# Optimization experiments

Hardware: AMD Instinct MI355X
Metric: run time of the kernel (lower is better)

The kernel has to match this reference:

```python
import jax, jax.numpy as jnp
import numpy as np

NUM_ROUTING = 3
EPS = 1e-8


def squash(s, axis=-1):
    # v = ||s||^2/(1+||s||^2) * s/||s||
    sq = jnp.sum(s * s, axis=axis, keepdims=True)
    return sq / (1.0 + sq) * s / (jnp.sqrt(sq) + EPS)


def setup_inputs() -> dict:
    key = jax.random.key(0)
    k1, k2 = jax.random.split(key)
    batch, in_caps, in_dim = 16, 2048, 64
    num_caps, dim_caps = 64, 32
    x = jax.random.normal(k1, (batch, in_caps, in_dim), dtype=jnp.float32)
    # learned transform W[j, d, k]  (torch shape (1,num_caps,1,dim_caps,in_dim) with singletons dropped)
    W = 0.01 * jax.random.normal(k2, (num_caps, dim_caps, in_dim), dtype=jnp.float32)
    return {"x": x, "W": W}


def reference(x, W):
    # u_hat[b,j,i,d] = sum_k W[j,d,k] * x[b,i,k]
    u_hat = jnp.einsum('jdk,bik->bjid', W, x)  # (b, num_caps, in_caps, dim_caps)
    u_hat_d = jax.lax.stop_gradient(u_hat)     # routing uses detached predictions

    b = jnp.zeros(u_hat.shape[:3] + (1,), dtype=u_hat.dtype)  # (b, J, I, 1)
    for _ in range(NUM_ROUTING - 1):
        c = jax.nn.softmax(b, axis=1)                # over output capsules J
        s = jnp.sum(c * u_hat_d, axis=2)             # (b, J, D)
        v = squash(s)
        # agreement uv[b,j,i] = <u_hat_d[b,j,i,:], v[b,j,:]>
        b = b + jnp.einsum('bjid,bjd->bji', u_hat_d, v)[..., None]

    c = jax.nn.softmax(b, axis=1)
    s = jnp.sum(c * u_hat, axis=2)
    return squash(s)  # (b, num_caps, dim_caps)
```

## Files before the change

kernel.cpp:

```cpp
#include <hip/hip_runtime.h>
#include <math.h>


#define BB 16
#define II 2048
#define KK 64
#define JJ 64
#define DD 32
#define ITILE 64
#define NT (II / ITILE)
#define YB 16

__global__ __launch_bounds__(256) void ybar_kernel(const float* __restrict__ x,
                                                   float* __restrict__ ybarp) {
    const int b = blockIdx.x;
    const int q = blockIdx.y;
    const int tid = threadIdx.x;
    const int kq = tid & 15;
    const int r  = tid >> 4;
    const float4* xp = (const float4*)(x + ((size_t)b * II + (size_t)q * 128) * KK) + kq;
    float4 a = make_float4(0.f, 0.f, 0.f, 0.f);
    #pragma unroll
    for (int n = 0; n < 8; ++n) {
        const float4 v = xp[(size_t)(r + n * 16) * 16];
        a.x += v.x; a.y += v.y; a.z += v.z; a.w += v.w;
    }
    __shared__ float4 sm[16][17];
    sm[r][kq] = a;
    __syncthreads();
    if (tid < 64) {
        const float* smf = (const float*)sm;
        float s = 0.f;
        #pragma unroll
        for (int rr = 0; rr < 16; ++rr) s += smf[rr * 68 + tid];
        ybarp[(b * YB + q) * KK + tid] = s * (1.0f / 64.0f);
    }
}

template <int MODE>
__global__ __launch_bounds__(256) void caps_kernel(const float* __restrict__ W,
                                                   const float* __restrict__ ybarp,
                                                   const float* __restrict__ ypart,
                                                   float* __restrict__ wv,
                                                   float* __restrict__ out) {
    const int b = blockIdx.x;
    const int jq = blockIdx.y;
    const int tid = threadIdx.x;
    const int w = tid >> 6;
    const int lane = tid & 63;
    const int j = jq * 4 + w;

    __shared__ alignas(16) float W_sm[4][DD][68];
    __shared__ alignas(16) float y_sm[4][KK];
    __shared__ float v_sm[4][DD];

    const float* Wp = W + (size_t)j * DD * KK;
    #pragma unroll
    for (int rr = 0; rr < 8; ++rr) {
        const int idx = rr * 64 + lane;
        const int d = idx >> 4, kq = idx & 15;
        *(float4*)&W_sm[w][d][kq * 4] = *(const float4*)(Wp + d * KK + kq * 4);
    }

    if (MODE == 0) {
        const float* yp = ybarp + (size_t)b * YB * KK + lane;
        float a = 0.f;
        #pragma unroll
        for (int t = 0; t < YB; ++t) a += yp[(size_t)t * KK];
        y_sm[w][lane] = a;
    } else {
        const int kq = lane & 15, th = lane >> 4;
        float4 a = make_float4(0.f, 0.f, 0.f, 0.f);
        #pragma unroll
        for (int n = 0; n < 8; ++n) {
            const int t = th + n * 4;
            const float4 v = *(const float4*)(ypart +
                (((size_t)b * NT + t) * JJ + j) * KK + kq * 4);
            a.x += v.x; a.y += v.y; a.z += v.z; a.w += v.w;
        }
        a.x += __shfl_xor(a.x, 16, 64); a.y += __shfl_xor(a.y, 16, 64);
        a.z += __shfl_xor(a.z, 16, 64); a.w += __shfl_xor(a.w, 16, 64);
        a.x += __shfl_xor(a.x, 32, 64); a.y += __shfl_xor(a.y, 32, 64);
        a.z += __shfl_xor(a.z, 32, 64); a.w += __shfl_xor(a.w, 32, 64);
        if (lane < 16) *(float4*)&y_sm[w][kq * 4] = a;
    }

    const int d = lane & 31;
    const int kh = (lane >> 5) * 32;
    float sv = 0.f;
    #pragma unroll
    for (int kq = 0; kq < 8; ++kq) {
        const float4 wr = *(const float4*)&W_sm[w][d][kh + kq * 4];
        const float4 yr = *(const float4*)&y_sm[w][kh + kq * 4];
        sv += wr.x * yr.x + wr.y * yr.y + wr.z * yr.z + wr.w * yr.w;
    }
    sv += __shfl_xor(sv, 32, 64);

    float ps = sv * sv;
    #pragma unroll
    for (int m = 1; m < 32; m <<= 1) ps += __shfl_xor(ps, m, 64);
    const float f = ps / ((1.f + ps) * (sqrtf(ps) + 1e-8f));

    if (MODE == 2) {
        if (lane < DD) out[((size_t)b * JJ + j) * DD + lane] = sv * f;
    } else {
        if (lane < DD) v_sm[w][lane] = sv * f;
        float a = 0.f;
        #pragma unroll
        for (int dd = 0; dd < DD; ++dd) a += W_sm[w][dd][lane] * v_sm[w][dd];
        const size_t idx = ((size_t)b * JJ + j) * KK + lane;
        if (MODE == 1) a += wv[idx];
        wv[idx] = a;
    }
}

__global__ __launch_bounds__(256) void route_kernel(const float* __restrict__ x,
                                                    const float* __restrict__ wv,
                                                    float* __restrict__ ypart) {
    const int b = blockIdx.x;
    const int t = blockIdx.y;
    const int tid = threadIdx.x;
    const int i0 = t * ITILE;

    __shared__ alignas(16) float x_smT[KK][68];
    __shared__ alignas(16) float wv_smT[KK][68];
    __shared__ alignas(16) float uv_smT[JJ][68];
    __shared__ float red[8][72];

    const float4* x4 = (const float4*)(x + ((size_t)b * II + i0) * KK);
    #pragma unroll
    for (int n = 0; n < 4; ++n) {
        const int idx = tid + n * 256;
        const int i = idx >> 4, kq = idx & 15;
        const float4 v = x4[idx];
        x_smT[kq * 4 + 0][i] = v.x;
        x_smT[kq * 4 + 1][i] = v.y;
        x_smT[kq * 4 + 2][i] = v.z;
        x_smT[kq * 4 + 3][i] = v.w;
    }
    const float4* wv4 = (const float4*)(wv + (size_t)b * JJ * KK);
    #pragma unroll
    for (int n = 0; n < 4; ++n) {
        const int idx = tid + n * 256;
        const int jj = idx >> 4, kq = idx & 15;
        const float4 v = wv4[idx];
        wv_smT[kq * 4 + 0][jj] = v.x;
        wv_smT[kq * 4 + 1][jj] = v.y;
        wv_smT[kq * 4 + 2][jj] = v.z;
        wv_smT[kq * 4 + 3][jj] = v.w;
    }
    __syncthreads();

    {
        const int ib = (tid & 15) * 4, jb = (tid >> 4) * 4;
        float acc[4][4] = {};
        for (int k = 0; k < KK; ++k) {
            const float4 xv = *(const float4*)&x_smT[k][ib];
            const float4 wvv = *(const float4*)&wv_smT[k][jb];
            acc[0][0] += xv.x * wvv.x; acc[0][1] += xv.x * wvv.y;
            acc[0][2] += xv.x * wvv.z; acc[0][3] += xv.x * wvv.w;
            acc[1][0] += xv.y * wvv.x; acc[1][1] += xv.y * wvv.y;
            acc[1][2] += xv.y * wvv.z; acc[1][3] += xv.y * wvv.w;
            acc[2][0] += xv.z * wvv.x; acc[2][1] += xv.z * wvv.y;
            acc[2][2] += xv.z * wvv.z; acc[2][3] += xv.z * wvv.w;
            acc[3][0] += xv.w * wvv.x; acc[3][1] += xv.w * wvv.y;
            acc[3][2] += xv.w * wvv.z; acc[3][3] += xv.w * wvv.w;
        }
        #pragma unroll
        for (int r = 0; r < 4; ++r)
            *(float4*)&uv_smT[jb + r][ib] =
                make_float4(acc[0][r], acc[1][r], acc[2][r], acc[3][r]);
    }
    __syncthreads();

    {
        const int i = tid & 63;
        const int w = tid >> 6;
        const int j0 = w * 16;
        float e[16];
        float m = -1e30f;
        #pragma unroll
        for (int jj = 0; jj < 16; ++jj) {
            e[jj] = uv_smT[j0 + jj][i];
            m = fmaxf(m, e[jj]);
        }
        red[w][i] = m;
        __syncthreads();
        m = fmaxf(fmaxf(red[0][i], red[1][i]), fmaxf(red[2][i], red[3][i]));
        float s = 0.f;
        #pragma unroll
        for (int jj = 0; jj < 16; ++jj) {
            e[jj] = __expf(e[jj] - m);
            s += e[jj];
        }
        red[4 + w][i] = s;
        __syncthreads();
        const float inv = 1.f / (red[4][i] + red[5][i] + red[6][i] + red[7][i]);
        #pragma unroll
        for (int jj = 0; jj < 16; ++jj) uv_smT[j0 + jj][i] = e[jj] * inv;
    }
    __syncthreads();

    {
        const int a = tid & 15;
        const int kb = (tid >> 4) * 4;
        float acc[4][4] = {};
        for (int i = 0; i < ITILE; i += 4) {
            float4 xv[4];
            #pragma unroll
            for (int c = 0; c < 4; ++c) xv[c] = *(const float4*)&x_smT[kb + c][i];
            #pragma unroll
            for (int r = 0; r < 4; ++r) {
                const float4 cv = *(const float4*)&uv_smT[a + 16 * r][i];
                #pragma unroll
                for (int c = 0; c < 4; ++c)
                    acc[r][c] += cv.x * xv[c].x + cv.y * xv[c].y +
                                 cv.z * xv[c].z + cv.w * xv[c].w;
            }
        }
        float* yp = ypart + ((size_t)b * NT + t) * JJ * KK;
        #pragma unroll
        for (int r = 0; r < 4; ++r)
            *(float4*)&yp[(a + 16 * r) * KK + kb] =
                make_float4(acc[r][0], acc[r][1], acc[r][2], acc[r][3]);
    }
}

extern "C" void kernel_launch(void* const* d_in, const int* in_sizes, int n_in,
                              void* d_out, int out_size, void* d_ws, size_t ws_size,
                              hipStream_t stream) {
    const float* x = (const float*)d_in[0];
    const float* W = (const float*)d_in[1];
    float* out = (float*)d_out;
    float* ws = (float*)d_ws;

    float* wv    = ws;
    float* ybarp = ws + 65536;
    float* ypart = ws + 65536 + 16384;

    ybar_kernel<<<dim3(BB, YB), 256, 0, stream>>>(x, ybarp);
    caps_kernel<0><<<dim3(BB, 16), 256, 0, stream>>>(W, ybarp, ypart, wv, out);
    route_kernel<<<dim3(BB, NT), 256, 0, stream>>>(x, wv, ypart);
    caps_kernel<1><<<dim3(BB, 16), 256, 0, stream>>>(W, ybarp, ypart, wv, out);
    route_kernel<<<dim3(BB, NT), 256, 0, stream>>>(x, wv, ypart);
    caps_kernel<2><<<dim3(BB, 16), 256, 0, stream>>>(W, ybarp, ypart, wv, out);
}
```

Baseline: 96.71 us.

## Use bf16 MFMA for routing GEMMs with in-register softmax

Rewrites route_kernel so both small GEMMs (agreement logits x·wv and c^T·x) run on bf16 16x16x32 MFMA instructions instead of scalar FP32 FMA loops. x and wv are converted to bf16 in shared memory, and x is kept in both row and transposed layouts. The softmax over the 64 output capsules is done in registers with cross-lane shuffles, which drops two barriers and the shared reduction buffer. In exchange, routing logits and coupling coefficients are computed in bf16, which lowers precision, and the final ypart stores are scalar with a strided pattern.

New measurement: 82.03 us. 15.2% less time.

```diff
diff --git a/kernel.cpp b/kernel.cpp
--- a/kernel.cpp
+++ b/kernel.cpp
@@ -10,6 +10,15 @@
 #define ITILE 64
 #define NT (II / ITILE)
 #define YB 16
+
+typedef float f32x4 __attribute__((ext_vector_type(4)));
+typedef short bf16x8 __attribute__((ext_vector_type(8)));
+
+__device__ __forceinline__ unsigned short f2bf(float f) {
+    unsigned int u = __float_as_uint(f);
+    u += 0x7FFFu + ((u >> 16) & 1u);
+    return (unsigned short)(u >> 16);
+}
 
 __global__ __launch_bounds__(256) void ybar_kernel(const float* __restrict__ x,
                                                    float* __restrict__ ybarp) {
@@ -114,121 +123,121 @@
     }
 }
 
-__global__ __launch_bounds__(256) void route_kernel(const float* __restrict__ x,
-                                                    const float* __restrict__ wv,
-                                                    float* __restrict__ ypart) {
+#define RPAD 72
+
+__global__ __launch_bounds__(256, 4) void route_kernel(const float* __restrict__ x,
+                                                       const float* __restrict__ wv,
+                                                       float* __restrict__ ypart) {
     const int b = blockIdx.x;
     const int t = blockIdx.y;
     const int tid = threadIdx.x;
-    const int i0 = t * ITILE;
-
-    __shared__ alignas(16) float x_smT[KK][68];
-    __shared__ alignas(16) float wv_smT[KK][68];
-    __shared__ alignas(16) float uv_smT[JJ][68];
-    __shared__ float red[8][72];
-
-    const float4* x4 = (const float4*)(x + ((size_t)b * II + i0) * KK);
+    const int w = tid >> 6;
+    const int lr = tid & 15;
+    const int lg = (tid >> 4) & 3;
+
+    __shared__ unsigned short x_bf[64][RPAD];
+    __shared__ unsigned short xT_bf[64][RPAD];
+    __shared__ unsigned short wv_bf[64][RPAD];
+    __shared__ unsigned short c_bf[64][RPAD];
+
+    const float4* x4 = (const float4*)(x + ((size_t)b * II + t * ITILE) * KK);
     #pragma unroll
     for (int n = 0; n < 4; ++n) {
         const int idx = tid + n * 256;
         const int i = idx >> 4, kq = idx & 15;
         const float4 v = x4[idx];
-        x_smT[kq * 4 + 0][i] = v.x;
-        x_smT[kq * 4 + 1][i] = v.y;
-        x_smT[kq * 4 + 2][i] = v.z;
-        x_smT[kq * 4 + 3][i] = v.w;
+        const unsigned short b0 = f2bf(v.x), b1 = f2bf(v.y),
+                             b2 = f2bf(v.z), b3 = f2bf(v.w);
+        *(unsigned int*)&x_bf[i][kq * 4 + 0] = (unsigned int)b0 | ((unsigned int)b1 << 16);
+        *(unsigned int*)&x_bf[i][kq * 4 + 2] = (unsigned int)b2 | ((unsigned int)b3 << 16);
+        xT_bf[kq * 4 + 0][i] = b0;
+        xT_bf[kq * 4 + 1][i] = b1;
+        xT_bf[kq * 4 + 2][i] = b2;
+        xT_bf[kq * 4 + 3][i] = b3;
     }
     const float4* wv4 = (const float4*)(wv + (size_t)b * JJ * KK);
     #pragma unroll
     for (int n = 0; n < 4; ++n) {
         const int idx = tid + n * 256;
-        const int jj = idx >> 4, kq = idx & 15;
+        const int j = idx >> 4, kq = idx & 15;
         const float4 v = wv4[idx];
-        wv_smT[kq * 4 + 0][jj] = v.x;
-        wv_smT[kq * 4 + 1][jj] = v.y;
-        wv_smT[kq * 4 + 2][jj] = v.z;
-        wv_smT[kq * 4 + 3][jj] = v.w;
+        *(unsigned int*)&wv_bf[j][kq * 4 + 0] =
+            (unsigned int)f2bf(v.x) | ((unsigned int)f2bf(v.y) << 16);
+        *(unsigned int*)&wv_bf[j][kq * 4 + 2] =
+            (unsigned int)f2bf(v.z) | ((unsigned int)f2bf(v.w) << 16);
     }
     __syncthreads();
 
+    f32x4 acc[4] = {{0,0,0,0},{0,0,0,0},{0,0,0,0},{0,0,0,0}};
     {
-        const int ib = (tid & 15) * 4, jb = (tid >> 4) * 4;
-        float acc[4][4] = {};
-        for (int k = 0; k < KK; ++k) {
-            const float4 xv = *(const float4*)&x_smT[k][ib];
-            const float4 wvv = *(const float4*)&wv_smT[k][jb];
-            acc[0][0] += xv.x * wvv.x; acc[0][1] += xv.x * wvv.y;
-            acc[0][2] += xv.x * wvv.z; acc[0][3] += xv.x * wvv.w;
-            acc[1][0] += xv.y * wvv.x; acc[1][1] += xv.y * wvv.y;
-            acc[1][2] += xv.y * wvv.z; acc[1][3] += xv.y * wvv.w;
-            acc[2][0] += xv.z * wvv.x; acc[2][1] += xv.z * wvv.y;
-            acc[2][2] += xv.z * wvv.z; acc[2][3] += xv.z * wvv.w;
-            acc[3][0] += xv.w * wvv.x; acc[3][1] += xv.w * wvv.y;
-            acc[3][2] += xv.w * wvv.z; acc[3][3] += xv.w * wvv.w;
-        }
+        const bf16x8 a0 = *(const bf16x8*)&x_bf[16 * w + lr][lg * 8];
+        const bf16x8 a1 = *(const bf16x8*)&x_bf[16 * w + lr][32 + lg * 8];
+        #pragma unroll
+        for (int jt = 0; jt < 4; ++jt) {
+            const bf16x8 bf0 = *(const bf16x8*)&wv_bf[jt * 16 + lr][lg * 8];
+            const bf16x8 bf1 = *(const bf16x8*)&wv_bf[jt * 16 + lr][32 + lg * 8];
+            acc[jt] = __builtin_amdgcn_mfma_f32_16x16x32_bf16(a0, bf0, acc[jt], 0, 0, 0);
+            acc[jt] = __builtin_amdgcn_mfma_f32_16x16x32_bf16(a1, bf1, acc[jt], 0, 0, 0);
+        }
+    }
+
+    float c[4][4];
+    #pragma unroll
+    for (int r = 0; r < 4; ++r) {
+        float m = fmaxf(fmaxf(acc[0][r], acc[1][r]), fmaxf(acc[2][r], acc[3][r]));
+        m = fmaxf(m, __shfl_xor(m, 1, 64));
+        m = fmaxf(m, __shfl_xor(m, 2, 64));
+        m = fmaxf(m, __shfl_xor(m, 4, 64));
+        m = fmaxf(m, __shfl_xor(m, 8, 64));
+        const float e0 = __expf(acc[0][r] - m);
+        const float e1 = __expf(acc[1][r] - m);
+        const float e2 = __expf(acc[2][r] - m);
+        const float e3 = __expf(acc[3][r] - m);
+        float s = e0 + e1 + e2 + e3;
+        s += __shfl_xor(s, 1, 64);
+        s += __shfl_xor(s, 2, 64);
+        s += __shfl_xor(s, 4, 64);
+        s += __shfl_xor(s, 8, 64);
+        const float inv = 1.f / s;
+        c[0][r] = e0 * inv; c[1][r] = e1 * inv;
+        c[2][r] = e2 * inv; c[3][r] = e3 * inv;
+    }
+
+    #pragma unroll
+    for (int jt = 0; jt < 4; ++jt) {
+        #pragma unroll
+        for (int rp = 0; rp < 2; ++rp) {
+            const unsigned int pk = (unsigned int)f2bf(c[jt][rp * 2])
+                                  | ((unsigned int)f2bf(c[jt][rp * 2 + 1]) << 16);
+            *(unsigned int*)&c_bf[jt * 16 + lr][16 * w + lg * 4 + rp * 2] = pk;
+        }
+    }
+    __syncthreads();
+
+    f32x4 acy[4] = {{0,0,0,0},{0,0,0,0},{0,0,0,0},{0,0,0,0}};
+    {
+        const bf16x8 c0 = *(const bf16x8*)&c_bf[16 * w + lr][lg * 8];
+        const bf16x8 c1 = *(const bf16x8*)&c_bf[16 * w + lr][32 + lg * 8];
+        #pragma unroll
+        for (int kt = 0; kt < 4; ++kt) {
+            const bf16x8 xf0 = *(const bf16x8*)&xT_bf[kt * 16 + lr][lg * 8];
+            const bf16x8 xf1 = *(const bf16x8*)&xT_bf[kt * 16 + lr][32 + lg * 8];
+            acy[kt] = __builtin_amdgcn_mfma_f32_16x16x32_bf16(c0, xf0, acy[kt], 0, 0, 0);
+            acy[kt] = __builtin_amdgcn_mfma_f32_16x16x32_bf16(c1, xf1, acy[kt], 0, 0, 0);
+        }
+    }
+    float* yp = ypart + ((size_t)b * NT + t) * JJ * KK;
+    #pragma unroll
+    for (int kt = 0; kt < 4; ++kt)
         #pragma unroll
         for (int r = 0; r < 4; ++r)
-            *(float4*)&uv_smT[jb + r][ib] =
-                make_float4(acc[0][r], acc[1][r], acc[2][r], acc[3][r]);
-    }
-    __syncthreads();
-
-    {
-        const int i = tid & 63;
-        const int w = tid >> 6;
-        const int j0 = w * 16;
-        float e[16];
-        float m = -1e30f;
-        #pragma unroll
-        for (int jj = 0; jj < 16; ++jj) {
-            e[jj] = uv_smT[j0 + jj][i];
-            m = fmaxf(m, e[jj]);
-        }
-        red[w][i] = m;
-        __syncthreads();
-        m = fmaxf(fmaxf(red[0][i], red[1][i]), fmaxf(red[2][i], red[3][i]));
-        float s = 0.f;
-        #pragma unroll
-        for (int jj = 0; jj < 16; ++jj) {
-            e[jj] = __expf(e[jj] - m);
-            s += e[jj];
-        }
-        red[4 + w][i] = s;
-        __syncthreads();
-        const float inv = 1.f / (red[4][i] + red[5][i] + red[6][i] + red[7][i]);
-        #pragma unroll
-        for (int jj = 0; jj < 16; ++jj) uv_smT[j0 + jj][i] = e[jj] * inv;
-    }
-    __syncthreads();
-
-    {
-        const int a = tid & 15;
-        const int kb = (tid >> 4) * 4;
-        float acc[4][4] = {};
-        for (int i = 0; i < ITILE; i += 4) {
-            float4 xv[4];
-            #pragma unroll
-            for (int c = 0; c < 4; ++c) xv[c] = *(const float4*)&x_smT[kb + c][i];
-            #pragma unroll
-            for (int r = 0; r < 4; ++r) {
-                const float4 cv = *(const float4*)&uv_smT[a + 16 * r][i];
-                #pragma unroll
-                for (int c = 0; c < 4; ++c)
-                    acc[r][c] += cv.x * xv[c].x + cv.y * xv[c].y +
-                                 cv.z * xv[c].z + cv.w * xv[c].w;
-            }
-        }
-        float* yp = ypart + ((size_t)b * NT + t) * JJ * KK;
-        #pragma unroll
-        for (int r = 0; r < 4; ++r)
-            *(float4*)&yp[(a + 16 * r) * KK + kb] =
-                make_float4(acc[r][0], acc[r][1], acc[r][2], acc[r][3]);
-    }
+            yp[(16 * w + lg * 4 + r) * KK + kt * 16 + lr] = acy[kt][r];
 }
 
 extern "C" void kernel_launch(void* const* d_in, const int* in_sizes, int n_in,
                               void* d_out, int out_size, void* d_ws, size_t ws_size,
                               hipStream_t stream) {
+    (void)in_sizes; (void)n_in; (void)out_size; (void)ws_size;
     const float* x = (const float*)d_in[0];
     const float* W = (const float*)d_in[1];
     float* out = (float*)d_out;
```
